# Optimization experiments

Measured on AMD Instinct MI355X. Metric: run time of the kernel, lower is better.

## Reference

```python
import jax, jax.numpy as jnp
import numpy as np

N_TOK, BATCH, D, MEM, H, W = 196, 64, 256, 2048, 16, 16


def setup_inputs() -> dict:
    key = jax.random.key(0)
    ks = jax.random.split(key, 9)
    w_scale = 1.0 / np.sqrt(D)  # ~ Linear default init scale
    return {
        "input_tokens": jax.random.normal(ks[0], (N_TOK, BATCH, D), jnp.float32),
        "ch_memory": jax.random.normal(ks[1], (MEM, D), jnp.float32) * 0.1,
        "ch_wq": jax.random.normal(ks[2], (D, D), jnp.float32) * w_scale,
        "ch_wk": jax.random.normal(ks[3], (D, D), jnp.float32) * w_scale,
        "ch_wv": jax.random.normal(ks[4], (D, D), jnp.float32) * w_scale,
        "sp_memory": jax.random.normal(ks[5], (MEM, H, W), jnp.float32) * 0.1,
        "sp_wq": jax.random.normal(ks[6], (D, D), jnp.float32) * w_scale,
        "sp_wk": jax.random.normal(ks[7], (D, D), jnp.float32) * w_scale,
        "sp_wv": jax.random.normal(ks[8], (D, D), jnp.float32) * w_scale,
    }


def reference(input_tokens, ch_memory, ch_wq, ch_wk, ch_wv,
              sp_memory, sp_wq, sp_wk, sp_wv):
    n_tok, batch, d = input_tokens.shape
    hw = d  # spatial branch requires feature_dim == H*W
    x = input_tokens.reshape(n_tok * batch, d)  # [NB, D]

    # ---- Channel memory branch: dot-product softmax read ----
    q = x @ ch_wq.T                       # [NB, D]
    k = ch_memory @ ch_wk.T               # [M, D]
    v = ch_memory @ ch_wv.T               # [M, D]
    scores = (q @ k.T) * (1.0 / jnp.sqrt(jnp.float32(d)))  # [NB, M]
    att_c = jax.nn.softmax(scores, axis=-1)
    out_c = att_c @ v                     # [NB, D]

    # ---- Spatial memory branch: SSIM-score softmax read ----
    mem_flat = sp_memory.reshape(sp_memory.shape[0], hw)  # [M, HW]
    qf = x @ sp_wq.T                      # [NB, HW]
    kf = mem_flat @ sp_wk.T               # [M, HW]
    vf = mem_flat @ sp_wv.T               # [M, HW]

    q_mean = jnp.mean(qf, axis=1, keepdims=True)          # [NB, 1]
    k_mean = jnp.mean(kf, axis=1, keepdims=True)          # [M, 1]
    q_var = jnp.var(qf, axis=1, ddof=1, keepdims=True)    # unbiased, like torch.var
    k_var = jnp.var(kf, axis=1, ddof=1, keepdims=True)
    cov = ((qf - q_mean) @ (kf - k_mean).T) / jnp.float32(hw - 1)  # [NB, M]

    c1, c2 = 0.01, 0.03
    mean_prod = q_mean @ k_mean.T                          # [NB, M]
    numerator = (2.0 * mean_prod + c1) * (2.0 * cov + c2)
    denominator = (q_mean ** 2 + (k_mean.T) ** 2 + c1) * (q_var + k_var.T + c2)
    ssim = numerator / (denominator + 1e-8)                # [NB, M]

    att_s = jax.nn.softmax(ssim, axis=-1)
    out_s = att_s @ vf                     # [NB, HW] == [NB, D]

    return (out_c + out_s).reshape(n_tok, batch, d)
```

## Files before the change

kernel.cpp:

```cpp
#include <hip/hip_runtime.h>

#define NBQ 12544
#define DM  256
#define MM  2048

typedef __attribute__((ext_vector_type(8)))  __bf16 bf16x8;
typedef __attribute__((ext_vector_type(4)))  float  floatx4;

__device__ __forceinline__ ushort f2bf(float x) {
    unsigned u = __float_as_uint(x);
    u += 0x7fffu + ((u >> 16) & 1u);
    return (ushort)(u >> 16);
}
__device__ __forceinline__ float bf2f(ushort h) {
    return __uint_as_float(((unsigned)h) << 16);
}

__global__ __launch_bounds__(256) void gemm_proj_all(
    const float* __restrict__ x,      const float* __restrict__ ch_mem,
    const float* __restrict__ ch_wq,  const float* __restrict__ ch_wk,
    const float* __restrict__ ch_wv,  const float* __restrict__ sp_mem,
    const float* __restrict__ sp_wq,  const float* __restrict__ sp_wk,
    const float* __restrict__ sp_wv,
    ushort* __restrict__ Qb,  ushort* __restrict__ QFb,
    ushort* __restrict__ Kb,  ushort* __restrict__ KFb,
    ushort* __restrict__ Vtb, ushort* __restrict__ VFtb)
{
    __shared__ ushort As[64][72];
    __shared__ ushort W1s[64][72];
    __shared__ ushort W2s[64][72];

    int bid = blockIdx.x;
    const float* A; const float* W1; const float* W2;
    ushort* C1; ushort* C2; int nrows, trans2;
    if (bid < 784) {
        A = x; W1 = ch_wq; W2 = sp_wq; C1 = Qb; C2 = QFb; nrows = NBQ; trans2 = 0;
    } else if (bid < 912) {
        A = ch_mem; W1 = ch_wk; W2 = ch_wv; C1 = Kb; C2 = Vtb;
        nrows = MM; trans2 = 1; bid -= 784;
    } else {
        A = sp_mem; W1 = sp_wk; W2 = sp_wv; C1 = KFb; C2 = VFtb;
        nrows = MM; trans2 = 1; bid -= 912;
    }
    const int r0 = (bid >> 2) * 64;
    const int c0 = (bid & 3) * 64;

    const int tid  = threadIdx.x;
    const int wv   = tid >> 6;
    const int lane = tid & 63;
    const int quad = lane >> 4;
    const int l16  = lane & 15;
    const int rw = (wv & 1) * 32;
    const int cw = (wv >> 1) * 32;

    floatx4 acc1[2][2], acc2[2][2];
    #pragma unroll
    for (int i = 0; i < 2; ++i)
        #pragma unroll
        for (int j = 0; j < 2; ++j) {
            acc1[i][j] = (floatx4){0.f, 0.f, 0.f, 0.f};
            acc2[i][j] = (floatx4){0.f, 0.f, 0.f, 0.f};
        }

    for (int d0 = 0; d0 < 256; d0 += 64) {
        __syncthreads();
        #pragma unroll
        for (int it = 0; it < 4; ++it) {
            int idx = tid + it * 256;
            int r = idx >> 4, c4 = (idx & 15) * 4;
            float4 a4 = *(const float4*)(A  + (size_t)(r0 + r) * 256 + d0 + c4);
            float4 w14 = *(const float4*)(W1 + (size_t)(c0 + r) * 256 + d0 + c4);
            float4 w24 = *(const float4*)(W2 + (size_t)(c0 + r) * 256 + d0 + c4);
            ushort4 ab, w1b, w2b;
            ab.x = f2bf(a4.x);  ab.y = f2bf(a4.y);  ab.z = f2bf(a4.z);  ab.w = f2bf(a4.w);
            w1b.x = f2bf(w14.x); w1b.y = f2bf(w14.y); w1b.z = f2bf(w14.z); w1b.w = f2bf(w14.w);
            w2b.x = f2bf(w24.x); w2b.y = f2bf(w24.y); w2b.z = f2bf(w24.z); w2b.w = f2bf(w24.w);
            *(ushort4*)&As[r][c4]  = ab;
            *(ushort4*)&W1s[r][c4] = w1b;
            *(ushort4*)&W2s[r][c4] = w2b;
        }
        __syncthreads();
        #pragma unroll
        for (int kk = 0; kk < 64; kk += 32) {
            bf16x8 aA0 = *(const bf16x8*)&As[rw + l16][kk + quad * 8];
            bf16x8 aA1 = *(const bf16x8*)&As[rw + 16 + l16][kk + quad * 8];
            bf16x8 b10 = *(const bf16x8*)&W1s[cw + l16][kk + quad * 8];
            bf16x8 b11 = *(const bf16x8*)&W1s[cw + 16 + l16][kk + quad * 8];
            bf16x8 b20 = *(const bf16x8*)&W2s[cw + l16][kk + quad * 8];
            bf16x8 b21 = *(const bf16x8*)&W2s[cw + 16 + l16][kk + quad * 8];
            acc1[0][0] = __builtin_amdgcn_mfma_f32_16x16x32_bf16(aA0, b10, acc1[0][0], 0, 0, 0);
            acc1[0][1] = __builtin_amdgcn_mfma_f32_16x16x32_bf16(aA0, b11, acc1[0][1], 0, 0, 0);
            acc1[1][0] = __builtin_amdgcn_mfma_f32_16x16x32_bf16(aA1, b10, acc1[1][0], 0, 0, 0);
            acc1[1][1] = __builtin_amdgcn_mfma_f32_16x16x32_bf16(aA1, b11, acc1[1][1], 0, 0, 0);
            acc2[0][0] = __builtin_amdgcn_mfma_f32_16x16x32_bf16(aA0, b20, acc2[0][0], 0, 0, 0);
            acc2[0][1] = __builtin_amdgcn_mfma_f32_16x16x32_bf16(aA0, b21, acc2[0][1], 0, 0, 0);
            acc2[1][0] = __builtin_amdgcn_mfma_f32_16x16x32_bf16(aA1, b20, acc2[1][0], 0, 0, 0);
            acc2[1][1] = __builtin_amdgcn_mfma_f32_16x16x32_bf16(aA1, b21, acc2[1][1], 0, 0, 0);
        }
    }

    #pragma unroll
    for (int ag = 0; ag < 2; ++ag)
        #pragma unroll
        for (int cg = 0; cg < 2; ++cg)
            #pragma unroll
            for (int i = 0; i < 4; ++i)
                C1[(size_t)(r0 + rw + ag * 16 + quad * 4 + i) * 256
                   + c0 + cw + cg * 16 + l16] = f2bf(acc1[ag][cg][i]);

    if (!trans2) {
        #pragma unroll
        for (int ag = 0; ag < 2; ++ag)
            #pragma unroll
            for (int cg = 0; cg < 2; ++cg)
                #pragma unroll
                for (int i = 0; i < 4; ++i)
                    C2[(size_t)(r0 + rw + ag * 16 + quad * 4 + i) * 256
                       + c0 + cw + cg * 16 + l16] = f2bf(acc2[ag][cg][i]);
    } else {
        __syncthreads();
        #pragma unroll
        for (int ag = 0; ag < 2; ++ag)
            #pragma unroll
            for (int cg = 0; cg < 2; ++cg)
                #pragma unroll
                for (int i = 0; i < 4; ++i)
                    W2s[cw + cg * 16 + l16][rw + ag * 16 + quad * 4 + i] = f2bf(acc2[ag][cg][i]);
        __syncthreads();
        const int col = tid >> 2;
        const int seg = (tid & 3) * 16;
        #pragma unroll
        for (int j = 0; j < 2; ++j)
            *(uint4*)(C2 + (size_t)(c0 + col) * nrows + r0 + seg + j * 8) =
                *(const uint4*)&W2s[col][seg + j * 8];
    }
}

__global__ __launch_bounds__(256) void row_stats_kf(
    const ushort* __restrict__ KFb, float* __restrict__ km, float* __restrict__ kv)
{
    const int row  = blockIdx.x * 4 + (threadIdx.x >> 6);
    const int lane = threadIdx.x & 63;
    ushort4 u = *(const ushort4*)(KFb + (size_t)row * 256 + lane * 4);
    float a = bf2f(u.x), b = bf2f(u.y), c = bf2f(u.z), d = bf2f(u.w);
    float s  = a + b + c + d;
    float ss = a * a + b * b + c * c + d * d;
    #pragma unroll
    for (int off = 32; off > 0; off >>= 1) {
        s  += __shfl_down(s, off);
        ss += __shfl_down(ss, off);
    }
    if (lane == 0) {
        float m = s * (1.f / 256.f);
        km[row] = m;
        kv[row] = (ss - 256.f * m * m) * (1.f / 255.f);
    }
}

__global__ __launch_bounds__(256, 2) void fused_attn_st(
    const ushort* __restrict__ Qb,  const ushort* __restrict__ QFb,
    const ushort* __restrict__ Kb,  const ushort* __restrict__ KFb,
    const ushort* __restrict__ Vtb, const ushort* __restrict__ VFtb,
    const float* __restrict__ km_, const float* __restrict__ kv_,
    float* __restrict__ out)
{
    __shared__ ushort SM[37376];
    ushort (*K_lds)[264]  = (ushort(*)[264])(SM);
    ushort (*KF_lds)[264] = (ushort(*)[264])(SM + 8448);
    ushort (*Vt_lds)[40]  = (ushort(*)[40])(SM + 16896);
    ushort (*VFt_lds)[40] = (ushort(*)[40])(SM + 27136);
    float* combuf = (float*)(SM + 16896);

    const int tid  = threadIdx.x;
    const int wv   = tid >> 6;
    const int lane = tid & 63;
    const int quad = lane >> 4;
    const int l16  = lane & 15;
    const int qsel = wv & 1;
    const int br   = wv >> 1;
    const int q0   = blockIdx.x * 32;

    const ushort* qsrc = br ? QFb : Qb;
    bf16x8 aQ[8];
    {
        const ushort* qp = qsrc + (size_t)(q0 + qsel * 16 + l16) * DM + quad * 8;
        #pragma unroll
        for (int s = 0; s < 8; ++s) aQ[s] = *(const bf16x8*)(qp + s * 32);
    }

    float qmv = 0.f, qvv = 0.f;
    if (br) {
        float sum = 0.f, ss = 0.f;
        #pragma unroll
        for (int s = 0; s < 8; ++s)
            #pragma unroll
            for (int j = 0; j < 8; ++j) {
                float v = (float)aQ[s][j];
                sum += v; ss += v * v;
            }
        sum += __shfl_xor(sum, 16, 64); sum += __shfl_xor(sum, 32, 64);
        ss  += __shfl_xor(ss, 16, 64);  ss  += __shfl_xor(ss, 32, 64);
        qmv = sum * (1.f / 256.f);
        qvv = (ss - 256.f * qmv * qmv) * (1.f / 255.f);
    }

    floatx4 acc[16];
    #pragma unroll
    for (int t = 0; t < 16; ++t) acc[t] = (floatx4){0.f, 0.f, 0.f, 0.f};
    float den = 0.f;

    for (int kt = 0; kt < MM; kt += 32) {
        __syncthreads();
        #pragma unroll
        for (int it = 0; it < 4; ++it) {
            int idx = tid + it * 256;
            int r = idx >> 5, c8 = (idx & 31) * 8;
            int pr = ((r & 4) << 2) | ((r >> 3) << 2) | (r & 3);
            *(uint4*)&K_lds[pr][c8]  = *(const uint4*)(Kb  + (size_t)(kt + r) * DM + c8);
            *(uint4*)&KF_lds[pr][c8] = *(const uint4*)(KFb + (size_t)(kt + r) * DM + c8);
        }
        #pragma unroll
        for (int it = 0; it < 4; ++it) {
            int idx = tid + it * 256;
            int d = idx >> 2, kc = (idx & 3) * 8;
            *(uint4*)&Vt_lds[d][kc]  = *(const uint4*)(Vtb  + (size_t)d * MM + kt + kc);
            *(uint4*)&VFt_lds[d][kc] = *(const uint4*)(VFtb + (size_t)d * MM + kt + kc);
        }
        __syncthreads();

        floatx4 S0 = (floatx4){0.f, 0.f, 0.f, 0.f};
        floatx4 S1 = (floatx4){0.f, 0.f, 0.f, 0.f};
        const ushort (*Ksrc)[264] = br ? KF_lds : K_lds;
        #pragma unroll
        for (int s = 0; s < 8; ++s) {
            bf16x8 aK0 = *(const bf16x8*)&Ksrc[l16][s * 32 + quad * 8];
            bf16x8 aK1 = *(const bf16x8*)&Ksrc[16 + l16][s * 32 + quad * 8];
            S0 = __builtin_amdgcn_mfma_f32_16x16x32_bf16(aK0, aQ[s], S0, 0, 0, 0);
            S1 = __builtin_amdgcn_mfma_f32_16x16x32_bf16(aK1, aQ[s], S1, 0, 0, 0);
        }

        float p[8];
        if (!br) {
            #pragma unroll
            for (int r = 0; r < 4; ++r) {
                p[r]     = __expf(S0[r] * 0.0625f);
                p[4 + r] = __expf(S1[r] * 0.0625f);
            }
        } else {
            floatx4 km0 = *(const floatx4*)(km_ + kt + 8 * quad);
            floatx4 km1 = *(const floatx4*)(km_ + kt + 8 * quad + 4);
            floatx4 kv0 = *(const floatx4*)(kv_ + kt + 8 * quad);
            floatx4 kv1 = *(const floatx4*)(kv_ + kt + 8 * quad + 4);
            #pragma unroll
            for (int r = 0; r < 4; ++r) {
                {
                    float mp  = qmv * km0[r];
                    float cov = (S0[r] - 256.f * mp) * (1.f / 255.f);
                    float num = (2.f * mp + 0.01f) * (2.f * cov + 0.03f);
                    float dn  = (qmv * qmv + km0[r] * km0[r] + 0.01f) * (qvv + kv0[r] + 0.03f);
                    p[r] = __expf(num / (dn + 1e-8f));
                }
                {
                    float mp  = qmv * km1[r];
                    float cov = (S1[r] - 256.f * mp) * (1.f / 255.f);
                    float num = (2.f * mp + 0.01f) * (2.f * cov + 0.03f);
                    float dn  = (qmv * qmv + km1[r] * km1[r] + 0.01f) * (qvv + kv1[r] + 0.03f);
                    p[4 + r] = __expf(num / (dn + 1e-8f));
                }
            }
        }
        union { ushort u[8]; bf16x8 v; } ap;
        #pragma unroll
        for (int j = 0; j < 8; ++j) {
            den += p[j];
            ap.u[j] = f2bf(p[j]);
        }

        const ushort (*Vsrc)[40] = br ? VFt_lds : Vt_lds;
        #pragma unroll
        for (int t = 0; t < 16; ++t) {
            bf16x8 bV = *(const bf16x8*)&Vsrc[t * 16 + l16][quad * 8];
            acc[t] = __builtin_amdgcn_mfma_f32_16x16x32_bf16(ap.v, bV, acc[t], 0, 0, 0);
        }
    }

    den += __shfl_xor(den, 16, 64);
    den += __shfl_xor(den, 32, 64);
    float rdn[4];
    #pragma unroll
    for (int r = 0; r < 4; ++r)
        rdn[r] = 1.f / __shfl(den, quad * 4 + r, 64);

    __syncthreads();
    if (br) {
        #pragma unroll
        for (int t = 0; t < 16; ++t)
            #pragma unroll
            for (int r = 0; r < 4; ++r)
                combuf[(qsel * 16 + quad * 4 + r) * 256 + t * 16 + l16] = acc[t][r] * rdn[r];
    }
    __syncthreads();
    if (!br) {
        #pragma unroll
        for (int t = 0; t < 16; ++t)
            #pragma unroll
            for (int r = 0; r < 4; ++r) {
                int ql = qsel * 16 + quad * 4 + r;
                out[(size_t)(q0 + ql) * DM + t * 16 + l16] =
                    acc[t][r] * rdn[r] + combuf[ql * 256 + t * 16 + l16];
            }
    }
}

extern "C" void kernel_launch(void* const* d_in, const int* in_sizes, int n_in,
                              void* d_out, int out_size, void* d_ws, size_t ws_size,
                              hipStream_t stream)
{
    const float* x      = (const float*)d_in[0];
    const float* ch_mem = (const float*)d_in[1];
    const float* ch_wq  = (const float*)d_in[2];
    const float* ch_wk  = (const float*)d_in[3];
    const float* ch_wv  = (const float*)d_in[4];
    const float* sp_mem = (const float*)d_in[5];
    const float* sp_wq  = (const float*)d_in[6];
    const float* sp_wk  = (const float*)d_in[7];
    const float* sp_wv  = (const float*)d_in[8];
    float* out = (float*)d_out;

    ushort* Qb   = (ushort*)d_ws;
    ushort* QFb  = Qb   + (size_t)NBQ * DM;
    ushort* Kb   = QFb  + (size_t)NBQ * DM;
    ushort* KFb  = Kb   + (size_t)MM * DM;
    ushort* Vtb  = KFb  + (size_t)MM * DM;
    ushort* VFtb = Vtb  + (size_t)MM * DM;
    float*  km   = (float*)(VFtb + (size_t)MM * DM);
    float*  kv   = km + MM;

    dim3 blk(256);
    gemm_proj_all<<<dim3(1040), blk, 0, stream>>>(
        x, ch_mem, ch_wq, ch_wk, ch_wv, sp_mem, sp_wq, sp_wk, sp_wv,
        Qb, QFb, Kb, KFb, Vtb, VFtb);
    row_stats_kf<<<dim3(MM / 4), blk, 0, stream>>>(KFb, km, kv);
    fused_attn_st<<<dim3(NBQ / 32), blk, 0, stream>>>(
        Qb, QFb, Kb, KFb, Vtb, VFtb, km, kv, out);
}
```

Baseline: 266.0 us.

## Split attention over memory halves with direct global-to-LDS loads and combine pass

Loads K/KF/Vt/VFt tiles straight into LDS with global_load_lds and XOR-swizzled layouts, replacing the register-staged copies and padded arrays. When the workspace is large enough, each query block's 2048-entry memory sweep is split into two halves run as separate blocks. Each half writes unnormalized partial outputs and denominators, and a new combine kernel sums and normalizes them. This doubles the grid to fill the GPU better and cuts per-block loop length, at the cost of roughly 50MB of extra partial-buffer traffic and an extra launch.

New measurement: 287.9 us. 1.08x slower.

```diff
diff --git a/kernel.cpp b/kernel.cpp
--- a/kernel.cpp
+++ b/kernel.cpp
@@ -14,6 +14,12 @@
 }
 __device__ __forceinline__ float bf2f(ushort h) {
     return __uint_as_float(((unsigned)h) << 16);
+}
+
+__device__ __forceinline__ void glds16(const ushort* g, ushort* l) {
+    __builtin_amdgcn_global_load_lds(
+        (const __attribute__((address_space(1))) unsigned int*)g,
+        (__attribute__((address_space(3))) unsigned int*)l, 16, 0, 0);
 }
 
 __global__ __launch_bounds__(256) void gemm_proj_all(
@@ -157,19 +163,16 @@
     }
 }
 
+template<int NHALF>
 __global__ __launch_bounds__(256, 2) void fused_attn_st(
     const ushort* __restrict__ Qb,  const ushort* __restrict__ QFb,
     const ushort* __restrict__ Kb,  const ushort* __restrict__ KFb,
     const ushort* __restrict__ Vtb, const ushort* __restrict__ VFtb,
     const float* __restrict__ km_, const float* __restrict__ kv_,
-    float* __restrict__ out)
+    float* __restrict__ out, float* __restrict__ part, float* __restrict__ denp)
 {
-    __shared__ ushort SM[37376];
-    ushort (*K_lds)[264]  = (ushort(*)[264])(SM);
-    ushort (*KF_lds)[264] = (ushort(*)[264])(SM + 8448);
-    ushort (*Vt_lds)[40]  = (ushort(*)[40])(SM + 16896);
-    ushort (*VFt_lds)[40] = (ushort(*)[40])(SM + 27136);
-    float* combuf = (float*)(SM + 16896);
+    __shared__ ushort SMu[32768];
+    float* combuf = (float*)SMu;
 
     const int tid  = threadIdx.x;
     const int wv   = tid >> 6;
@@ -178,7 +181,13 @@
     const int l16  = lane & 15;
     const int qsel = wv & 1;
     const int br   = wv >> 1;
-    const int q0   = blockIdx.x * 32;
+
+    const int bid   = blockIdx.x;
+    const int half  = (NHALF == 2) ? (bid & 1) : 0;
+    const int qc    = (NHALF == 2) ? (bid >> 1) : bid;
+    const int q0    = qc * 32;
+    const int kbase = half * (MM / NHALF);
+    const int NT    = (MM / NHALF) / 32;
 
     const ushort* qsrc = br ? QFb : Qb;
     bf16x8 aQ[8];
@@ -204,53 +213,70 @@
         qvv = (ss - 256.f * qmv * qmv) * (1.f / 255.f);
     }
 
+    int offK[4], offV[4];
+    #pragma unroll
+    for (int p = 0; p < 4; ++p) {
+        int j  = wv * 4 + p;
+        int Rk = 2 * j + (lane >> 5);
+        int rk = (Rk & 3) + ((Rk >> 4) & 1) * 4 + ((Rk >> 2) & 3) * 8;
+        int ck = (lane & 31) ^ (Rk & 7);
+        offK[p] = rk * DM + ck * 8;
+        int Rv = 16 * j + (lane >> 2);
+        int cv = (lane & 3) ^ (Rv & 3);
+        offV[p] = Rv * MM + cv * 8;
+    }
+
+    const ushort* kp  = Kb   + (size_t)kbase * DM;
+    const ushort* kfp = KFb  + (size_t)kbase * DM;
+    const ushort* vp  = Vtb  + kbase;
+    const ushort* vfp = VFtb + kbase;
+
     floatx4 acc[16];
     #pragma unroll
     for (int t = 0; t < 16; ++t) acc[t] = (floatx4){0.f, 0.f, 0.f, 0.f};
     float den = 0.f;
 
-    for (int kt = 0; kt < MM; kt += 32) {
-        __syncthreads();
-        #pragma unroll
-        for (int it = 0; it < 4; ++it) {
-            int idx = tid + it * 256;
-            int r = idx >> 5, c8 = (idx & 31) * 8;
-            int pr = ((r & 4) << 2) | ((r >> 3) << 2) | (r & 3);
-            *(uint4*)&K_lds[pr][c8]  = *(const uint4*)(Kb  + (size_t)(kt + r) * DM + c8);
-            *(uint4*)&KF_lds[pr][c8] = *(const uint4*)(KFb + (size_t)(kt + r) * DM + c8);
-        }
-        #pragma unroll
-        for (int it = 0; it < 4; ++it) {
-            int idx = tid + it * 256;
-            int d = idx >> 2, kc = (idx & 3) * 8;
-            *(uint4*)&Vt_lds[d][kc]  = *(const uint4*)(Vtb  + (size_t)d * MM + kt + kc);
-            *(uint4*)&VFt_lds[d][kc] = *(const uint4*)(VFtb + (size_t)d * MM + kt + kc);
-        }
-        __syncthreads();
-
+    const int ksw  = l16 & 7;
+    const int vswo = (quad ^ (l16 & 3)) * 8;
+
+    for (int ti = 0; ti < NT; ++ti) {
+        __syncthreads();
+        #pragma unroll
+        for (int p = 0; p < 4; ++p) {
+            int db = (wv * 4 + p) * 512;
+            glds16(kp  + offK[p], SMu + db);
+            glds16(kfp + offK[p], SMu + 8192 + db);
+            glds16(vp  + offV[p], SMu + 16384 + db);
+            glds16(vfp + offV[p], SMu + 24576 + db);
+        }
+        kp += 32 * DM; kfp += 32 * DM; vp += 32; vfp += 32;
+        __syncthreads();
+
+        const ushort* Ks = SMu + (br ? 8192 : 0);
         floatx4 S0 = (floatx4){0.f, 0.f, 0.f, 0.f};
         floatx4 S1 = (floatx4){0.f, 0.f, 0.f, 0.f};
-        const ushort (*Ksrc)[264] = br ? KF_lds : K_lds;
         #pragma unroll
         for (int s = 0; s < 8; ++s) {
-            bf16x8 aK0 = *(const bf16x8*)&Ksrc[l16][s * 32 + quad * 8];
-            bf16x8 aK1 = *(const bf16x8*)&Ksrc[16 + l16][s * 32 + quad * 8];
+            int off = (((s * 4 + quad) ^ ksw)) * 8;
+            bf16x8 aK0 = *(const bf16x8*)(Ks + l16 * DM + off);
+            bf16x8 aK1 = *(const bf16x8*)(Ks + 4096 + l16 * DM + off);
             S0 = __builtin_amdgcn_mfma_f32_16x16x32_bf16(aK0, aQ[s], S0, 0, 0, 0);
             S1 = __builtin_amdgcn_mfma_f32_16x16x32_bf16(aK1, aQ[s], S1, 0, 0, 0);
         }
 
-        float p[8];
+        const int kk = kbase + ti * 32;
+        float pb[8];
         if (!br) {
             #pragma unroll
             for (int r = 0; r < 4; ++r) {
-                p[r]     = __expf(S0[r] * 0.0625f);
-                p[4 + r] = __expf(S1[r] * 0.0625f);
+                pb[r]     = __expf(S0[r] * 0.0625f);
+                pb[4 + r] = __expf(S1[r] * 0.0625f);
             }
         } else {
-            floatx4 km0 = *(const floatx4*)(km_ + kt + 8 * quad);
-            floatx4 km1 = *(const floatx4*)(km_ + kt + 8 * quad + 4);
-            floatx4 kv0 = *(const floatx4*)(kv_ + kt + 8 * quad);
-            floatx4 kv1 = *(const floatx4*)(kv_ + kt + 8 * quad + 4);
+            floatx4 km0 = *(const floatx4*)(km_ + kk + 8 * quad);
+            floatx4 km1 = *(const floatx4*)(km_ + kk + 8 * quad + 4);
+            floatx4 kv0 = *(const floatx4*)(kv_ + kk + 8 * quad);
+            floatx4 kv1 = *(const floatx4*)(kv_ + kk + 8 * quad + 4);
             #pragma unroll
             for (int r = 0; r < 4; ++r) {
                 {
@@ -258,57 +284,95 @@
                     float cov = (S0[r] - 256.f * mp) * (1.f / 255.f);
                     float num = (2.f * mp + 0.01f) * (2.f * cov + 0.03f);
                     float dn  = (qmv * qmv + km0[r] * km0[r] + 0.01f) * (qvv + kv0[r] + 0.03f);
-                    p[r] = __expf(num / (dn + 1e-8f));
+                    pb[r] = __expf(num / (dn + 1e-8f));
                 }
                 {
                     float mp  = qmv * km1[r];
                     float cov = (S1[r] - 256.f * mp) * (1.f / 255.f);
                     float num = (2.f * mp + 0.01f) * (2.f * cov + 0.03f);
                     float dn  = (qmv * qmv + km1[r] * km1[r] + 0.01f) * (qvv + kv1[r] + 0.03f);
-                    p[4 + r] = __expf(num / (dn + 1e-8f));
+                    pb[4 + r] = __expf(num / (dn + 1e-8f));
                 }
             }
         }
         union { ushort u[8]; bf16x8 v; } ap;
         #pragma unroll
         for (int j = 0; j < 8; ++j) {
-            den += p[j];
-            ap.u[j] = f2bf(p[j]);
-        }
-
-        const ushort (*Vsrc)[40] = br ? VFt_lds : Vt_lds;
+            den += pb[j];
+            ap.u[j] = f2bf(pb[j]);
+        }
+
+        const ushort* Vs = SMu + (br ? 24576 : 16384);
         #pragma unroll
         for (int t = 0; t < 16; ++t) {
-            bf16x8 bV = *(const bf16x8*)&Vsrc[t * 16 + l16][quad * 8];
+            bf16x8 bV = *(const bf16x8*)(Vs + (t * 16 + l16) * 32 + vswo);
             acc[t] = __builtin_amdgcn_mfma_f32_16x16x32_bf16(ap.v, bV, acc[t], 0, 0, 0);
         }
     }
 
     den += __shfl_xor(den, 16, 64);
     den += __shfl_xor(den, 32, 64);
-    float rdn[4];
-    #pragma unroll
-    for (int r = 0; r < 4; ++r)
-        rdn[r] = 1.f / __shfl(den, quad * 4 + r, 64);
-
-    __syncthreads();
-    if (br) {
+
+    if (NHALF == 1) {
+        float rdn[4];
+        #pragma unroll
+        for (int r = 0; r < 4; ++r)
+            rdn[r] = 1.f / __shfl(den, quad * 4 + r, 64);
+
+        __syncthreads();
+        if (br) {
+            #pragma unroll
+            for (int t = 0; t < 16; ++t)
+                #pragma unroll
+                for (int r = 0; r < 4; ++r)
+                    combuf[(qsel * 16 + quad * 4 + r) * 256 + t * 16 + l16] = acc[t][r] * rdn[r];
+        }
+        __syncthreads();
+        if (!br) {
+            #pragma unroll
+            for (int t = 0; t < 16; ++t)
+                #pragma unroll
+                for (int r = 0; r < 4; ++r) {
+                    int ql = qsel * 16 + quad * 4 + r;
+                    out[(size_t)(q0 + ql) * DM + t * 16 + l16] =
+                        acc[t][r] * rdn[r] + combuf[ql * 256 + t * 16 + l16];
+                }
+        }
+    } else {
+        float* Np = part + (size_t)(half * 2 + br) * ((size_t)NBQ * DM);
         #pragma unroll
         for (int t = 0; t < 16; ++t)
             #pragma unroll
             for (int r = 0; r < 4; ++r)
-                combuf[(qsel * 16 + quad * 4 + r) * 256 + t * 16 + l16] = acc[t][r] * rdn[r];
-    }
-    __syncthreads();
-    if (!br) {
-        #pragma unroll
-        for (int t = 0; t < 16; ++t)
-            #pragma unroll
-            for (int r = 0; r < 4; ++r) {
-                int ql = qsel * 16 + quad * 4 + r;
-                out[(size_t)(q0 + ql) * DM + t * 16 + l16] =
-                    acc[t][r] * rdn[r] + combuf[ql * 256 + t * 16 + l16];
-            }
+                Np[(size_t)(q0 + qsel * 16 + quad * 4 + r) * DM + t * 16 + l16] = acc[t][r];
+        if (lane < 16)
+            denp[(size_t)(half * 2 + br) * NBQ + q0 + qsel * 16 + lane] = den;
+    }
+}
+
+__global__ __launch_bounds__(256) void combine_halves(
+    const float* __restrict__ part, const float* __restrict__ denp,
+    float* __restrict__ out)
+{
+    const size_t stride = (size_t)NBQ * 64;
+    const float4* p4 = (const float4*)part;
+    float4* o4 = (float4*)out;
+    #pragma unroll
+    for (int u = 0; u < 2; ++u) {
+        size_t i = (size_t)blockIdx.x * 512 + (size_t)u * 256 + threadIdx.x;
+        int q = (int)(i >> 6);
+        float rc = 1.f / (denp[q] + denp[2 * NBQ + q]);
+        float rs = 1.f / (denp[NBQ + q] + denp[3 * NBQ + q]);
+        float4 c0 = p4[i];
+        float4 s0 = p4[stride + i];
+        float4 c1 = p4[2 * stride + i];
+        float4 s1 = p4[3 * stride + i];
+        float4 r;
+        r.x = (c0.x + c1.x) * rc + (s0.x + s1.x) * rs;
+        r.y = (c0.y + c1.y) * rc + (s0.y + s1.y) * rs;
+        r.z = (c0.z + c1.z) * rc + (s0.z + s1.z) * rs;
+        r.w = (c0.w + c1.w) * rc + (s0.w + s1.w) * rs;
+        o4[i] = r;
     }
 }
 
@@ -335,12 +399,25 @@
     ushort* VFtb = Vtb  + (size_t)MM * DM;
     float*  km   = (float*)(VFtb + (size_t)MM * DM);
     float*  kv   = km + MM;
+    float*  part = kv + MM;
+    float*  denp = part + (size_t)4 * NBQ * DM;
+
+    const size_t base_b = (2 * (size_t)NBQ * DM + 4 * (size_t)MM * DM) * sizeof(ushort)
+                        + 2 * (size_t)MM * sizeof(float);
+    const size_t need   = base_b + ((size_t)4 * NBQ * DM + 4 * NBQ) * sizeof(float);
+    const bool split = ws_size >= need;
 
     dim3 blk(256);
     gemm_proj_all<<<dim3(1040), blk, 0, stream>>>(
         x, ch_mem, ch_wq, ch_wk, ch_wv, sp_mem, sp_wq, sp_wk, sp_wv,
         Qb, QFb, Kb, KFb, Vtb, VFtb);
     row_stats_kf<<<dim3(MM / 4), blk, 0, stream>>>(KFb, km, kv);
-    fused_attn_st<<<dim3(NBQ / 32), blk, 0, stream>>>(
-        Qb, QFb, Kb, KFb, Vtb, VFtb, km, kv, out);
-}
+    if (split) {
+        fused_attn_st<2><<<dim3(2 * NBQ / 32), blk, 0, stream>>>(
+            Qb, QFb, Kb, KFb, Vtb, VFtb, km, kv, out, part, denp);
+        combine_halves<<<dim3(NBQ * DM / 4 / 512), blk, 0, stream>>>(part, denp, out);
+    } else {
+        fused_attn_st<1><<<dim3(NBQ / 32), blk, 0, stream>>>(
+            Qb, QFb, Kb, KFb, Vtb, VFtb, km, kv, out, part, denp);
+    }
+}
```
